# Optimization experiments

Hardware: AMD Instinct MI355X
Metric: run time of the kernel (lower is better)

Reference implementation:

```python
import jax, jax.numpy as jnp
import numpy as np

B, SL = 16, 512
S = SL - 1            # context length after shift (length=1)
E = 256               # embedding_size / hidden_size
NH = 4                # num_heads
K = 4                 # conv1d_kernel_size
I = 2 * E             # mLSTM inner dim (_inner_embedding_dim = 2*E)
DHM = I // NH         # mLSTM head dim
DHS = E // NH         # sLSTM head dim
NB, BS = I // 4, 4    # qkv_proj_blocksize=4 block-diagonal projections
F = 384               # gated FFN up dim = round_up(1.3*256, 64)
NUM_SKILLS, NUM_Q = 500, 10000
EPS = 1e-5


def _ln(x, w):
    mu = x.mean(-1, keepdims=True)
    var = x.var(-1, keepdims=True)
    return (x - mu) / jnp.sqrt(var + EPS) * w


def _causal_dwconv(x, w, b):
    # x: (B,S,C), depthwise causal conv with kernel (C,K)
    xt = jnp.transpose(x, (0, 2, 1))
    y = jax.lax.conv_general_dilated(
        xt, w[:, None, :], (1,), [(K - 1, 0)],
        dimension_numbers=('NCH', 'OIH', 'NCH'),
        feature_group_count=x.shape[-1])
    return jnp.transpose(y, (0, 2, 1)) + b


def _headwise(x, w):
    # block-diagonal linear: w (NB, BS, BS)
    xb = x.reshape(x.shape[0], x.shape[1], NB, BS)
    return jnp.einsum('bsnd,nod->bsno', xb, w).reshape(x.shape)


def _forward(questions, responses, skills,
             q_embed, qa_embed, q_embed_diff, qa_embed_diff, difficult_param,
             ln0_w, m_up_w, m_up_b, m_conv_w, m_conv_b, m_q_w, m_k_w, m_v_w,
             m_ig_w, m_ig_b, m_fg_w, m_fg_b, m_outnorm_w, m_skip, m_down_w, m_down_b,
             ln1_w, s_conv_w, s_conv_b, s_gate_w, s_rec_w, s_bias, s_gn_w,
             ln2_w, ffn_up_w, ffn_up_b, ffn_down_w, ffn_down_b,
             postnorm_w, out_w1, out_b1, out_w2, out_b2, out_w3, out_b3):
    pid = questions[:, :-1]
    q_data = skills[:, :-1]
    q_shft = skills[:, 1:]
    target = (responses * (responses > -1).astype(responses.dtype))[:, :-1]

    q_e = q_embed[q_data]                              # (B,S,E)
    qa_e = qa_embed[target] + q_e
    pid_e = difficult_param[pid]                       # (B,S,1)
    q_e = q_e + pid_e * q_embed_diff[q_data]
    qa_e = qa_e + pid_e * qa_embed_diff[target]

    # ---- xLSTM stack: block 0 = mLSTM block, block 1 = sLSTM block + gated FFN ----
    x = qa_e  # dropout is identity in eval

    # mLSTM block: x = x + mlstm_layer(LN(x))
    h = _ln(x, ln0_w)
    up = h @ m_up_w.T + m_up_b                         # (B,S,2I)
    x_m, z = jnp.split(up, 2, axis=-1)
    xc = jax.nn.silu(_causal_dwconv(x_m, m_conv_w, m_conv_b))
    q = _headwise(xc, m_q_w)
    k = _headwise(xc, m_k_w)
    v = _headwise(x_m, m_v_w)
    ifin = jnp.concatenate([q, k, v], axis=-1)         # (B,S,3I)
    ig = jnp.einsum('bsf,hf->bhs', ifin, m_ig_w) + m_ig_b[None, :, None]
    fg = jnp.einsum('bsf,hf->bhs', ifin, m_fg_w) + m_fg_b[None, :, None]
    qh = q.reshape(B, S, NH, DHM).transpose(0, 2, 1, 3)
    kh = k.reshape(B, S, NH, DHM).transpose(0, 2, 1, 3)
    vh = v.reshape(B, S, NH, DHM).transpose(0, 2, 1, 3)
    # parallel stabilized mLSTM
    logf = jax.nn.log_sigmoid(fg)                      # (B,NH,S)
    cs = jnp.concatenate([jnp.zeros((B, NH, 1), logf.dtype), jnp.cumsum(logf, -1)], -1)
    dmat = cs[:, :, 1:, None] - cs[:, :, None, 1:]     # (B,NH,S,S): sum of logf over (s,t]
    ltr = jnp.tril(jnp.ones((S, S), bool))
    logD = jnp.where(ltr, dmat, -jnp.inf) + ig[:, :, None, :]
    maxD = jnp.max(logD, -1, keepdims=True)
    D = jnp.exp(logD - maxD)
    qk = jnp.einsum('bhtd,bhsd->bhts', qh, kh) * (DHM ** -0.5)
    C = qk * D
    norm = jnp.maximum(jnp.abs(C.sum(-1, keepdims=True)), jnp.exp(-maxD))
    hh = jnp.einsum('bhts,bhsd->bhtd', C / (norm + 1e-6), vh)
    # multi-head layernorm (per head over DHM), weight on flattened dim
    hn = (hh - hh.mean(-1, keepdims=True)) / jnp.sqrt(hh.var(-1, keepdims=True) + EPS)
    hflat = hn.transpose(0, 2, 1, 3).reshape(B, S, I) * m_outnorm_w
    hout = (hflat + m_skip * xc) * jax.nn.silu(z)
    x = x + (hout @ m_down_w.T + m_down_b)

    # sLSTM block: x = x + slstm_layer(LN(x)); x = x + ffn(LN(x))
    h = _ln(x, ln1_w)
    hc = jax.nn.silu(_causal_dwconv(h, s_conv_w, s_conv_b))
    hh4 = h.reshape(B, S, NH, DHS)
    hc4 = hc.reshape(B, S, NH, DHS)
    gi = jnp.einsum('bsnd,nod->bsno', hc4, s_gate_w[0])   # i,f from conv path
    gf = jnp.einsum('bsnd,nod->bsno', hc4, s_gate_w[1])
    gz = jnp.einsum('bsnd,nod->bsno', hh4, s_gate_w[2])   # z,o from x path
    go = jnp.einsum('bsnd,nod->bsno', hh4, s_gate_w[3])
    wx = jnp.stack([gi, gf, gz, go], axis=2) + s_bias[None, None]  # (B,S,4,NH,DHS)

    def step(carry, wx_t):
        y, c, n, m = carry
        raw = wx_t + jnp.einsum('bnd,gnde->bgne', y, s_rec_w)
        iraw, fraw, zraw, oraw = raw[:, 0], raw[:, 1], raw[:, 2], raw[:, 3]
        logfplusm = m + jax.nn.log_sigmoid(fraw)
        mnew = jnp.maximum(iraw, logfplusm)
        ig_ = jnp.exp(iraw - mnew)
        fg_ = jnp.exp(logfplusm - mnew)
        cnew = fg_ * c + ig_ * jnp.tanh(zraw)
        nnew = fg_ * n + ig_
        ynew = jax.nn.sigmoid(oraw) * cnew / nnew
        return (ynew, cnew, nnew, mnew), ynew

    z0 = jnp.zeros((B, NH, DHS), x.dtype)
    _, ys = jax.lax.scan(step, (z0, z0, z0, z0), jnp.swapaxes(wx, 0, 1))
    y = jnp.swapaxes(ys, 0, 1)                           # (B,S,NH,DHS)
    yn = (y - y.mean(-1, keepdims=True)) / jnp.sqrt(y.var(-1, keepdims=True) + EPS)
    x = x + yn.reshape(B, S, E) * s_gn_w

    # gated FFN (relu)
    h = _ln(x, ln2_w)
    gate, upf = jnp.split(h @ ffn_up_w.T + ffn_up_b, 2, axis=-1)
    x = x + (jax.nn.relu(gate) * upf) @ ffn_down_w.T + ffn_down_b

    d = _ln(x, postnorm_w)                               # post_blocks_norm

    fam = jnp.where((target == 1)[..., None], d, 0.0)
    unfam = jnp.where((target == 0)[..., None], d, 0.0)
    d2 = d - pid_e
    cq = jnp.concatenate([d2, q_e, fam, unfam], axis=-1)  # (B,S,4E)
    o = jax.nn.relu(cq @ out_w1.T + out_b1)
    o = jax.nn.relu(o @ out_w2.T + out_b2)
    probs = jax.nn.sigmoid(o @ out_w3.T + out_b3)
    pred = jnp.take_along_axis(probs, q_shft[..., None], axis=-1)[..., 0]
    return pred                                          # (B,S)


def setup_inputs():
    key = jax.random.key(0)
    ks = iter(jax.random.split(key, 64))
    def rn(shape, s=0.02):
        return jax.random.normal(next(ks), shape, jnp.float32) * s
    return dict(
        questions=jax.random.randint(next(ks), (B, SL), 0, NUM_Q),
        responses=jax.random.randint(next(ks), (B, SL), 0, 2),
        skills=jax.random.randint(next(ks), (B, SL), 0, NUM_SKILLS),
        attention_mask=jnp.ones((B, SL), jnp.int32),
        q_embed=rn((NUM_SKILLS, E), 1.0),
        qa_embed=rn((2, E), 1.0),
        q_embed_diff=rn((NUM_SKILLS + 1, E), 1.0),
        qa_embed_diff=rn((2 * NUM_SKILLS + 1, E), 1.0),
        difficult_param=rn((NUM_Q + 1, 1), 0.1),
        ln0_w=jnp.ones((E,)),
        m_up_w=rn((2 * I, E)), m_up_b=jnp.zeros((2 * I,)),
        m_conv_w=rn((I, K), 0.1), m_conv_b=jnp.zeros((I,)),
        m_q_w=rn((NB, BS, BS), 0.1), m_k_w=rn((NB, BS, BS), 0.1), m_v_w=rn((NB, BS, BS), 0.1),
        m_ig_w=rn((NH, 3 * I)), m_ig_b=jnp.zeros((NH,)),
        m_fg_w=rn((NH, 3 * I)), m_fg_b=jnp.zeros((NH,)),
        m_outnorm_w=jnp.ones((I,)), m_skip=jnp.ones((I,)),
        m_down_w=rn((E, I)), m_down_b=jnp.zeros((E,)),
        ln1_w=jnp.ones((E,)),
        s_conv_w=rn((E, K), 0.1), s_conv_b=jnp.zeros((E,)),
        s_gate_w=rn((4, NH, DHS, DHS), 0.1),
        s_rec_w=rn((4, NH, DHS, DHS), 0.05),
        s_bias=jnp.zeros((4, NH, DHS)),
        s_gn_w=jnp.ones((E,)),
        ln2_w=jnp.ones((E,)),
        ffn_up_w=rn((2 * F, E)), ffn_up_b=jnp.zeros((2 * F,)),
        ffn_down_w=rn((E, F)), ffn_down_b=jnp.zeros((E,)),
        postnorm_w=jnp.ones((E,)),
        out_w1=rn((2 * E, 4 * E)), out_b1=jnp.zeros((2 * E,)),
        out_w2=rn((E, 2 * E)), out_b2=jnp.zeros((E,)),
        out_w3=rn((NUM_SKILLS, E)), out_b3=jnp.zeros((NUM_SKILLS,)),
    )


def reference(questions, responses, skills, attention_mask,
              q_embed, qa_embed, q_embed_diff, qa_embed_diff, difficult_param,
              ln0_w, m_up_w, m_up_b, m_conv_w, m_conv_b, m_q_w, m_k_w, m_v_w,
              m_ig_w, m_ig_b, m_fg_w, m_fg_b, m_outnorm_w, m_skip, m_down_w, m_down_b,
              ln1_w, s_conv_w, s_conv_b, s_gate_w, s_rec_w, s_bias, s_gn_w,
              ln2_w, ffn_up_w, ffn_up_b, ffn_down_w, ffn_down_b,
              postnorm_w, out_w1, out_b1, out_w2, out_b2, out_w3, out_b3):
    return _forward(questions, responses, skills,
                    q_embed, qa_embed, q_embed_diff, qa_embed_diff, difficult_param,
                    ln0_w, m_up_w, m_up_b, m_conv_w, m_conv_b, m_q_w, m_k_w, m_v_w,
                    m_ig_w, m_ig_b, m_fg_w, m_fg_b, m_outnorm_w, m_skip, m_down_w, m_down_b,
                    ln1_w, s_conv_w, s_conv_b, s_gate_w, s_rec_w, s_bias, s_gn_w,
                    ln2_w, ffn_up_w, ffn_up_b, ffn_down_w, ffn_down_b,
                    postnorm_w, out_w1, out_b1, out_w2, out_b2, out_w3, out_b3)
```

## Files before the change

### kernel.cpp

```cpp
#include <hip/hip_runtime.h>
#include <hip/hip_bf16.h>

#define B_    16
#define SL_   512
#define S_    511
#define E_    256
#define NH_   4
#define I_    512
#define DHM_  128
#define DHS_  64
#define F_    384
#define NP_   8192
#define NROW  (B_*S_)
#define EPS_  1e-5f

typedef __hip_bfloat16 bf16;
typedef __bf16 bf16x8v __attribute__((ext_vector_type(8)));
typedef float  f32x4v  __attribute__((ext_vector_type(4)));

__device__ __forceinline__ float rcp_(float x){ return __builtin_amdgcn_rcpf(x); }
__device__ __forceinline__ float sig_(float x){ return rcp_(1.f+__expf(-x)); }
__device__ __forceinline__ float silu_(float x){ return x*sig_(x); }
__device__ __forceinline__ float logsig_(float x){ return fminf(x,0.f) - __logf(1.f + __expf(-fabsf(x))); }
__device__ __forceinline__ float expneg_(float x){ return __expf(fminf(x,0.f)); }
__device__ __forceinline__ float expclamp_(float x){ return __expf(fminf(fmaxf(x,-80.f),80.f)); }
__device__ __forceinline__ float tanh_(float x){ return 1.f - 2.f*rcp_(__expf(2.f*x)+1.f); }

__global__ __launch_bounds__(256) void k_cvt16(const float* __restrict__ src, bf16* __restrict__ dst, int n){
  int i=blockIdx.x*256+threadIdx.x;
  if(i<n) dst[i]=__float2bfloat16(src[i]);
}
__global__ __launch_bounds__(256) void k_cvtsplit(const float* __restrict__ src,
  bf16* __restrict__ hi, bf16* __restrict__ lo, int n){
  int i=blockIdx.x*256+threadIdx.x;
  if(i<n){
    float v=src[i];
    bf16 h=__float2bfloat16(v);
    hi[i]=h;
    lo[i]=__float2bfloat16(v-__bfloat162float(h));
  }
}
__global__ __launch_bounds__(256) void k_wtrans(const float* __restrict__ src, float* __restrict__ dst){
  int i = blockIdx.x*256+threadIdx.x;
  int blk = i>>12;
  int d = (i>>6)&63;
  int e = i&63;
  dst[(size_t)(blk*64+d)*64+e] = src[(size_t)(blk*64+e)*64+d];
}

__global__ __launch_bounds__(256) void k_wfrag(const float* __restrict__ rw, bf16* __restrict__ wf){
  int i = blockIdx.x*256+threadIdx.x;
  int j  = i&7;
  int l  = (i>>3)&63;
  int kf = (i>>9)&1;
  int t  = (i>>10)&15;
  int n  = i>>14;
  int g = t>>2;
  int e = (t&3)*16 + (l&15);
  int d = (l>>4)*16 + kf*8 + j;
  wf[i] = __float2bfloat16(rw[((size_t)((g*4+n)*64 + d))*64 + e]);
}

__global__ __launch_bounds__(256) void k_embed(
  const int* __restrict__ questions, const int* __restrict__ responses, const int* __restrict__ skills,
  const float* __restrict__ q_embed, const float* __restrict__ qa_embed,
  const float* __restrict__ q_embed_diff, const float* __restrict__ qa_embed_diff,
  const float* __restrict__ difficult_param, const float* __restrict__ ln0w,
  float* __restrict__ x, float* __restrict__ qe,
  bf16* __restrict__ h_hi, bf16* __restrict__ h_lo,
  float* __restrict__ pide, int* __restrict__ tgt, int* __restrict__ qsh)
{
  __shared__ float red[256];
  int r = blockIdx.x; int e = threadIdx.x;
  float xa = 0.f;
  if (r < NROW){
    int b = r / S_, s = r % S_;
    int pid  = questions[b*SL_+s];
    int qd   = skills[b*SL_+s];
    int resp = responses[b*SL_+s];
    int t    = (resp > -1) ? resp : 0;
    float pe = difficult_param[pid];
    float q0 = q_embed[qd*E_+e];
    xa = q0 + qa_embed[t*E_+e] + pe*qa_embed_diff[t*E_+e];
    float qn = q0 + pe*q_embed_diff[qd*E_+e];
    x[(size_t)r*E_+e]=xa; qe[(size_t)r*E_+e]=qn;
    if (e==0){ pide[r]=pe; tgt[r]=t; qsh[r]=skills[b*SL_+s+1]; }
  } else {
    x[(size_t)r*E_+e]=0.f; qe[(size_t)r*E_+e]=0.f;
    if (e==0){ pide[r]=0.f; tgt[r]=-7; qsh[r]=0; }
  }
  red[e]=xa; __syncthreads();
  for(int s2=128;s2>0;s2>>=1){ if(e<s2) red[e]+=red[e+s2]; __syncthreads(); }
  float mu = red[0]*(1.f/E_); __syncthreads();
  float d = xa-mu;
  red[e]=d*d; __syncthreads();
  for(int s2=128;s2>0;s2>>=1){ if(e<s2) red[e]+=red[e+s2]; __syncthreads(); }
  float var = red[0]*(1.f/E_);
  float o = d*rsqrtf(var+EPS_)*ln0w[e];
  bf16 hv = __float2bfloat16(o);
  h_hi[(size_t)r*E_+e] = hv;
  h_lo[(size_t)r*E_+e] = __float2bfloat16(o-__bfloat162float(hv));
}

__global__ __launch_bounds__(256) void k_ln(
  const float* __restrict__ in, const float* __restrict__ w, float* __restrict__ out)
{
  __shared__ float red[256];
  int r = blockIdx.x, t = threadIdx.x;
  float v = in[(size_t)r*E_+t];
  red[t]=v; __syncthreads();
  for(int s=128;s>0;s>>=1){ if(t<s) red[t]+=red[t+s]; __syncthreads(); }
  float mu = red[0]*(1.f/E_); __syncthreads();
  float d = v-mu;
  red[t]=d*d; __syncthreads();
  for(int s=128;s>0;s>>=1){ if(t<s) red[t]+=red[t+s]; __syncthreads(); }
  float var = red[0]*(1.f/E_);
  out[(size_t)r*E_+t] = d*rsqrtf(var+EPS_)*w[t];
}

__global__ __launch_bounds__(256) void k_gemm16s(
  const bf16* __restrict__ Ah, const bf16* __restrict__ Al,
  const bf16* __restrict__ Bh, const bf16* __restrict__ Bl,
  const float* __restrict__ bias, float* __restrict__ C, int M, int K)
{
  int tid=threadIdx.x;
  int wave=tid>>6, lane=tid&63;
  int wr=wave>>1, wc=wave&1;
  int row0=blockIdx.y*64 + wr*32;
  int col0=blockIdx.x*64 + wc*32;
  int lrow = lane&15, lq = lane>>4;
  f32x4v acc[2][2] = {};
  size_t aoff = (size_t)(row0+lrow)*K + lq*8;
  size_t boff = (size_t)(col0+lrow)*K + lq*8;
  for(int k0=0;k0<K;k0+=32){
    bf16x8v ah0=*(const bf16x8v*)(Ah+aoff+k0), ah1=*(const bf16x8v*)(Ah+aoff+(size_t)16*K+k0);
    bf16x8v al0=*(const bf16x8v*)(Al+aoff+k0), al1=*(const bf16x8v*)(Al+aoff+(size_t)16*K+k0);
    bf16x8v bh0=*(const bf16x8v*)(Bh+boff+k0), bh1=*(const bf16x8v*)(Bh+boff+(size_t)16*K+k0);
    bf16x8v bl0=*(const bf16x8v*)(Bl+boff+k0), bl1=*(const bf16x8v*)(Bl+boff+(size_t)16*K+k0);
    acc[0][0]=__builtin_amdgcn_mfma_f32_16x16x32_bf16(ah0,bh0,acc[0][0],0,0,0);
    acc[0][1]=__builtin_amdgcn_mfma_f32_16x16x32_bf16(ah0,bh1,acc[0][1],0,0,0);
    acc[1][0]=__builtin_amdgcn_mfma_f32_16x16x32_bf16(ah1,bh0,acc[1][0],0,0,0);
    acc[1][1]=__builtin_amdgcn_mfma_f32_16x16x32_bf16(ah1,bh1,acc[1][1],0,0,0);
    acc[0][0]=__builtin_amdgcn_mfma_f32_16x16x32_bf16(ah0,bl0,acc[0][0],0,0,0);
    acc[0][1]=__builtin_amdgcn_mfma_f32_16x16x32_bf16(ah0,bl1,acc[0][1],0,0,0);
    acc[1][0]=__builtin_amdgcn_mfma_f32_16x16x32_bf16(ah1,bl0,acc[1][0],0,0,0);
    acc[1][1]=__builtin_amdgcn_mfma_f32_16x16x32_bf16(ah1,bl1,acc[1][1],0,0,0);
    acc[0][0]=__builtin_amdgcn_mfma_f32_16x16x32_bf16(al0,bh0,acc[0][0],0,0,0);
    acc[0][1]=__builtin_amdgcn_mfma_f32_16x16x32_bf16(al0,bh1,acc[0][1],0,0,0);
    acc[1][0]=__builtin_amdgcn_mfma_f32_16x16x32_bf16(al1,bh0,acc[1][0],0,0,0);
    acc[1][1]=__builtin_amdgcn_mfma_f32_16x16x32_bf16(al1,bh1,acc[1][1],0,0,0);
  }
  #pragma unroll
  for(int mi=0;mi<2;mi++){
    #pragma unroll
    for(int ni=0;ni<2;ni++){
      #pragma unroll
      for(int r=0;r<4;r++){
        int row=row0+mi*16+lq*4+r;
        int col=col0+ni*16+lrow;
        C[(size_t)row*M+col]=acc[mi][ni][r] + bias[col];
      }
    }
  }
}

__global__ __launch_bounds__(256) void k_gemm16(
  const bf16* __restrict__ A, const bf16* __restrict__ Bw,
  const float* __restrict__ bias, const float* __restrict__ resid,
  float* __restrict__ C, bf16* __restrict__ C16,
  int M, int K, int relu)
{
  int tid=threadIdx.x;
  int wave=tid>>6, lane=tid&63;
  int wr=wave>>1, wc=wave&1;
  int row0=blockIdx.y*64 + wr*32;
  int col0=blockIdx.x*64 + wc*32;
  int lrow = lane&15, lq = lane>>4;
  f32x4v acc[2][2] = {};
  const bf16* Abase = A  + (size_t)(row0+lrow)*K + lq*8;
  const bf16* Bbase = Bw + (size_t)(col0+lrow)*K + lq*8;
  for(int k0=0;k0<K;k0+=32){
    bf16x8v a0 = *(const bf16x8v*)(Abase + k0);
    bf16x8v a1 = *(const bf16x8v*)(Abase + (size_t)16*K + k0);
    bf16x8v b0 = *(const bf16x8v*)(Bbase + k0);
    bf16x8v b1 = *(const bf16x8v*)(Bbase + (size_t)16*K + k0);
    acc[0][0]=__builtin_amdgcn_mfma_f32_16x16x32_bf16(a0,b0,acc[0][0],0,0,0);
    acc[0][1]=__builtin_amdgcn_mfma_f32_16x16x32_bf16(a0,b1,acc[0][1],0,0,0);
    acc[1][0]=__builtin_amdgcn_mfma_f32_16x16x32_bf16(a1,b0,acc[1][0],0,0,0);
    acc[1][1]=__builtin_amdgcn_mfma_f32_16x16x32_bf16(a1,b1,acc[1][1],0,0,0);
  }
  #pragma unroll
  for(int mi=0;mi<2;mi++){
    #pragma unroll
    for(int ni=0;ni<2;ni++){
      #pragma unroll
      for(int r=0;r<4;r++){
        int row=row0+mi*16+lq*4+r;
        int col=col0+ni*16+lrow;
        float v=acc[mi][ni][r] + (bias? bias[col]:0.f);
        if(relu) v=fmaxf(v,0.f);
        if(resid) v += resid[(size_t)row*M+col];
        if(C)   C[(size_t)row*M+col]=v;
        if(C16) C16[(size_t)row*M+col]=__float2bfloat16(v);
      }
    }
  }
}

__global__ __launch_bounds__(256) void k_conv_silu(
  const float* __restrict__ in, int ild, const float* __restrict__ w, const float* __restrict__ bws,
  float* __restrict__ out, int old_, int C)
{
  int i = blockIdx.x*256 + threadIdx.x;
  int r = i / C, c = i % C;
  if (r >= NP_) return;
  float acc = 0.f;
  if (r < NROW) {
    int b=r/S_, s=r%S_;
    acc = bws[c];
    #pragma unroll
    for(int j=0;j<4;j++){
      int ss=s-3+j;
      if(ss>=0) acc += w[c*4+j] * in[(size_t)(b*S_+ss)*ild + c];
    }
    acc = silu_(acc);
  }
  out[(size_t)r*old_ + c] = acc;
}

__global__ __launch_bounds__(256) void k_headwise(
  const float* __restrict__ xc, const float* __restrict__ xm, int xmld,
  const float* __restrict__ wq, const float* __restrict__ wk, const float* __restrict__ wv,
  float* __restrict__ q, float* __restrict__ k, float* __restrict__ v)
{
  int i=blockIdx.x*256+threadIdx.x;
  int r=i/I_, c=i%I_;
  if(r>=NP_) return;
  size_t oi=(size_t)r*I_+c;
  if(r>=NROW){ q[oi]=0.f; k[oi]=0.f; v[oi]=0.f; return; }
  int n=c>>2, o=c&3;
  const float* xcr = xc + (size_t)r*I_ + n*4;
  const float* xmr = xm + (size_t)r*xmld + n*4;
  float aq=0.f, ak=0.f, av=0.f;
  #pragma unroll
  for(int d=0;d<4;d++){
    float xcv=xcr[d], xmv=xmr[d];
    aq += xcv*wq[(n*4+o)*4+d];
    ak += xcv*wk[(n*4+o)*4+d];
    av += xmv*wv[(n*4+o)*4+d];
  }
  q[oi]=aq; k[oi]=ak; v[oi]=av;
}

__global__ __launch_bounds__(256) void k_igfg(
  const float* __restrict__ q, const float* __restrict__ k, const float* __restrict__ v,
  const float* __restrict__ wig, const float* __restrict__ big,
  const float* __restrict__ wfg, const float* __restrict__ bfg,
  float* __restrict__ igb, float* __restrict__ fgb)
{
  int r=blockIdx.x;
  int wid=threadIdx.x>>6, lane=threadIdx.x&63;
  int b=r/S_, s=r%S_;
  for(int c=wid; c<8; c+=4){
    int h=c>>1; int isfg=c&1;
    const float* w = isfg? wfg : wig;
    float acc=0.f;
    for(int f=lane; f<1536; f+=64){
      float val = (f<512)? q[(size_t)r*512+f]
                : (f<1024)? k[(size_t)r*512+f-512]
                : v[(size_t)r*512+f-1024];
      acc += val*w[h*1536+f];
    }
    for(int m=32;m;m>>=1) acc+=__shfl_xor(acc,m,64);
    if(lane==0){
      if(isfg) fgb[(b*4+h)*512+s]=acc+bfg[h];
      else     igb[(b*4+h)*512+s]=acc+big[h];
    }
  }
}

__global__ __launch_bounds__(256) void k_decay(
  const float* __restrict__ igb, const float* __restrict__ fgb,
  float* __restrict__ cs1, float* __restrict__ g, float* __restrict__ M)
{
  int bh = blockIdx.x; int tid = threadIdx.x;
  __shared__ float buf[512];
  __shared__ float buf2[512];
  for (int s=tid; s<512; s+=256)
    buf[s] = (s<S_) ? logsig_(fgb[bh*512+s]) : 0.f;
  __syncthreads();
  for (int off=1; off<512; off<<=1){
    int s0=tid, s1=tid+256;
    float v0 = buf[s0] + ((s0>=off)? buf[s0-off] : 0.f);
    float v1 = buf[s1] + ((s1>=off)? buf[s1-off] : 0.f);
    __syncthreads();
    buf[s0]=v0; buf[s1]=v1;
    __syncthreads();
  }
  for (int s=tid; s<512; s+=256){
    float c = buf[s];
    if (s<S_){
      cs1[bh*512+s]=c;
      float gv = igb[bh*512+s]-c;
      g[bh*512+s]=gv;
      buf2[s]=gv;
    } else buf2[s] = -3.4e38f;
  }
  __syncthreads();
  for (int off=1; off<512; off<<=1){
    int s0=tid, s1=tid+256;
    float v0 = fmaxf(buf2[s0], (s0>=off)? buf2[s0-off] : -3.4e38f);
    float v1 = fmaxf(buf2[s1], (s1>=off)? buf2[s1-off] : -3.4e38f);
    __syncthreads();
    buf2[s0]=v0; buf2[s1]=v1;
    __syncthreads();
  }
  for (int s=tid; s<S_; s+=256) M[bh*512+s] = buf2[s];
}

#define TQ 32
#define TS 32
__global__ __launch_bounds__(256) void k_attn(
  const float* __restrict__ q, const float* __restrict__ k, const float* __restrict__ v,
  const float* __restrict__ cs1, const float* __restrict__ g, const float* __restrict__ M,
  const float* __restrict__ onw, float* __restrict__ hflat)
{
  __shared__ __align__(16) float qs[TQ][132];
  __shared__ __align__(16) float ks[TS][132];
  __shared__ __align__(16) float vs[TS][128];
  __shared__ float Sw[TQ][33];
  __shared__ float MtS[TQ], cssS[TQ], lsumS[TQ], gsS[TS];
  int tq = blockIdx.x, bh = blockIdx.y;
  int b = bh>>2, h = bh&3;
  int tid = threadIdx.x;
  int i = tid>>4, j = tid&15;
  int t0 = tq*TQ;
  {
    int row = tid>>3, c4 = (tid&7)*4;
    const float4* src = (const float4*)(q + (size_t)(b*S_ + t0 + row)*512 + h*128);
    float4* dst = (float4*)&qs[row][0];
    #pragma unroll
    for(int c=0;c<4;c++) dst[c4+c] = src[c4+c];
  }
  if (tid < TQ){
    int t = t0 + tid; int tc = (t<S_)? t : (S_-1);
    MtS[tid]  = M[bh*512 + tc];
    cssS[tid] = cs1[bh*512 + tc];
    lsumS[tid]= 0.f;
  }
  float o[2][8] = {};
  int t1 = min(t0+TQ, S_);
  int nst = (t1 + TS - 1)/TS;
  const float sc = 0.08838834764831843f;
  for (int st=0; st<nst; ++st){
    int s0 = st*TS;
    __syncthreads();
    {
      int row = tid>>3, c4 = (tid&7)*4;
      const float4* srck = (const float4*)(k + (size_t)(b*S_ + s0 + row)*512 + h*128);
      const float4* srcv = (const float4*)(v + (size_t)(b*S_ + s0 + row)*512 + h*128);
      float4* dk = (float4*)&ks[row][0];
      float4* dv = (float4*)&vs[row][0];
      #pragma unroll
      for(int c=0;c<4;c++){ dk[c4+c]=srck[c4+c]; dv[c4+c]=srcv[c4+c]; }
      if (tid < TS) gsS[tid] = g[bh*512 + s0 + tid];
    }
    __syncthreads();
    float a00=0,a01=0,a10=0,a11=0;
    {
      const float4* q0 = (const float4*)&qs[i*2][0];
      const float4* q1 = (const float4*)&qs[i*2+1][0];
      const float4* k0 = (const float4*)&ks[j][0];
      const float4* k1 = (const float4*)&ks[j+16][0];
      #pragma unroll
      for(int d4=0; d4<32; ++d4){
        float4 qa=q0[d4], qb=q1[d4], ka=k0[d4], kb=k1[d4];
        a00 += qa.x*ka.x+qa.y*ka.y+qa.z*ka.z+qa.w*ka.w;
        a01 += qa.x*kb.x+qa.y*kb.y+qa.z*kb.z+qa.w*kb.w;
        a10 += qb.x*ka.x+qb.y*ka.y+qb.z*ka.z+qb.w*ka.w;
        a11 += qb.x*kb.x+qb.y*kb.y+qb.z*kb.z+qb.w*kb.w;
      }
    }
    int tA = t0 + i*2, tB = tA+1;
    int sA = s0 + j,   sB = sA + 16;
    float gA = gsS[j], gB = gsS[j+16];
    float mA = MtS[i*2], mB = MtS[i*2+1];
    float w00 = (sA<=tA)? a00*sc*expneg_(gA-mA) : 0.f;
    float w01 = (sB<=tA)? a01*sc*expneg_(gB-mA) : 0.f;
    float w10 = (sA<=tB)? a10*sc*expneg_(gA-mB) : 0.f;
    float w11 = (sB<=tB)? a11*sc*expneg_(gB-mB) : 0.f;
    float r0 = w00+w01, r1 = w10+w11;
    #pragma unroll
    for(int msk=1; msk<16; msk<<=1){ r0 += __shfl_xor(r0,msk,16); r1 += __shfl_xor(r1,msk,16); }
    if (j==0){ lsumS[i*2] += r0; lsumS[i*2+1] += r1; }
    Sw[i*2][j]     = w00; Sw[i*2][j+16]   = w01;
    Sw[i*2+1][j]   = w10; Sw[i*2+1][j+16] = w11;
    __syncthreads();
    #pragma unroll 8
    for(int s=0;s<TS;s++){
      float w0 = Sw[i*2][s], w1 = Sw[i*2+1][s];
      float4 v0 = *(const float4*)&vs[s][j*4];
      float4 v1 = *(const float4*)&vs[s][64+j*4];
      o[0][0]+=w0*v0.x; o[0][1]+=w0*v0.y; o[0][2]+=w0*v0.z; o[0][3]+=w0*v0.w;
      o[0][4]+=w0*v1.x; o[0][5]+=w0*v1.y; o[0][6]+=w0*v1.z; o[0][7]+=w0*v1.w;
      o[1][0]+=w1*v0.x; o[1][1]+=w1*v0.y; o[1][2]+=w1*v0.z; o[1][3]+=w1*v0.w;
      o[1][4]+=w1*v1.x; o[1][5]+=w1*v1.y; o[1][6]+=w1*v1.z; o[1][7]+=w1*v1.w;
    }
  }
  __syncthreads();
  #pragma unroll
  for(int r=0;r<2;r++){
    int tl = i*2+r;
    int t = t0 + tl;
    float maxD = cssS[tl] + MtS[tl];
    float norm = fmaxf(fabsf(lsumS[tl]), expclamp_(-maxD));
    float scale = rcp_(norm+1e-6f);
    float sum=0.f;
    #pragma unroll
    for(int d=0;d<8;d++){ o[r][d]*=scale; sum+=o[r][d]; }
    #pragma unroll
    for(int msk=1; msk<16; msk<<=1) sum += __shfl_xor(sum,msk,16);
    float mu = sum*(1.f/128.f);
    float var=0.f;
    #pragma unroll
    for(int d=0;d<8;d++){ float dd=o[r][d]-mu; var+=dd*dd; }
    #pragma unroll
    for(int msk=1; msk<16; msk<<=1) var += __shfl_xor(var,msk,16);
    float rs = rsqrtf(var*(1.f/128.f)+EPS_);
    if (t < S_){
      float* dst = hflat + (size_t)(b*S_+t)*1024 + h*128;
      #pragma unroll
      for(int c=0;c<4;c++) dst[j*4+c]    = (o[r][c]  -mu)*rs*onw[h*128+j*4+c];
      #pragma unroll
      for(int c=0;c<4;c++) dst[64+j*4+c] = (o[r][4+c]-mu)*rs*onw[h*128+64+j*4+c];
    }
  }
}

__global__ __launch_bounds__(256) void k_hout(
  const float* __restrict__ A, const float* __restrict__ xc, const float* __restrict__ skip,
  bf16* __restrict__ out16)
{
  int i=blockIdx.x*256+threadIdx.x;
  int r=i/512, c=i%512;
  float hf=A[(size_t)r*1024+c];
  float z =A[(size_t)r*1024+512+c];
  out16[(size_t)r*512+c] = __float2bfloat16((hf + skip[c]*xc[(size_t)r*512+c]) * silu_(z));
}

#define WXR 64
__global__ __launch_bounds__(256,2) void k_wx(
  const float* __restrict__ h, const float* __restrict__ hc,
  const float* __restrict__ gwT, const float* __restrict__ gb,
  float* __restrict__ wx)
{
  int rt = blockIdx.x, g = blockIdx.y;
  int tid = threadIdx.x;
  int n = tid>>6, e = tid&63;
  const float* src = (g<2)? hc : h;
  __shared__ __align__(16) float hs[WXR][260];
  float W[64];
  #pragma unroll
  for(int d=0;d<64;d++) W[d] = gwT[(size_t)(((g*4+n)*64+d))*64 + e];
  float bias = gb[(g*4+n)*64+e];
  int row0 = rt*WXR;
  for(int idx=tid; idx<WXR*64; idx+=256){
    int rr = idx>>6, cc4 = (idx&63)*4;
    *(float4*)&hs[rr][cc4] = *(const float4*)(src + (size_t)(row0+rr)*256 + cc4);
  }
  __syncthreads();
  #pragma unroll 4
  for(int rr=0; rr<WXR; ++rr){
    int r = row0+rr;
    if (r>=NROW) break;
    const float* hrow = &hs[rr][n*64];
    float a0=0,a1=0,a2=0,a3=0;
    #pragma unroll
    for(int d=0;d<64;d+=4){
      float4 hv = *(const float4*)&hrow[d];
      a0+=hv.x*W[d]; a1+=hv.y*W[d+1]; a2+=hv.z*W[d+2]; a3+=hv.w*W[d+3];
    }
    int b=r/S_, s=r%S_;
    wx[(((size_t)(b*4+n)*512 + s)*256) + e*4 + g] = bias + ((a0+a1)+(a2+a3));
  }
}

__global__ __launch_bounds__(256,1) void k_scan(
  const float* __restrict__ wx, const bf16* __restrict__ wf, float* __restrict__ y_out)
{
  int bn = blockIdx.x; int b = bn>>2, n = bn&3;
  int tid = threadIdx.x;
  int w = tid>>6;
  int l = tid&63;
  int q = l>>4;
  int el = l&15;
  int e  = w*16 + el;

  __shared__ __align__(16) unsigned short ybuf[2][64];

  if (tid < 128) ((unsigned short*)ybuf)[tid] = 0;
  __syncthreads();

  bf16x8v Wf2[4][2];
  #pragma unroll
  for(int g=0; g<4; ++g){
    #pragma unroll
    for(int kf=0; kf<2; ++kf){
      Wf2[g][kf] = *(const bf16x8v*)(wf + ((size_t)((n*16 + (4*g+w))*2 + kf)*64 + l)*8);
    }
  }

  const float* wxBase = wx + ((size_t)bn*512)*256 + e*4;
  float* yst = y_out + (size_t)(b*S_)*256 + n*64 + e;

  float4 p0,p1,p2,p3;
  p0 = *(const float4*)(wxBase + (size_t)0*256);
  p1 = *(const float4*)(wxBase + (size_t)1*256);
  p2 = *(const float4*)(wxBase + (size_t)2*256);
  p3 = *(const float4*)(wxBase + (size_t)3*256);

  f32x4v z4 = {0.f,0.f,0.f,0.f};
  float c=0.f, nn=0.f, pm=1.f;

  for (int s=0; s<S_; ++s){
    int p = s&1;
    bf16x8v a0 = *(const bf16x8v*)&ybuf[p][16*q];
    bf16x8v a1 = *(const bf16x8v*)&ybuf[p][16*q+8];

    f32x4v acc0,acc1,acc2,acc3;
    acc0 = __builtin_amdgcn_mfma_f32_16x16x32_bf16(a0, Wf2[0][0], z4, 0,0,0);
    acc1 = __builtin_amdgcn_mfma_f32_16x16x32_bf16(a0, Wf2[1][0], z4, 0,0,0);
    acc2 = __builtin_amdgcn_mfma_f32_16x16x32_bf16(a0, Wf2[2][0], z4, 0,0,0);
    acc3 = __builtin_amdgcn_mfma_f32_16x16x32_bf16(a0, Wf2[3][0], z4, 0,0,0);
    acc0 = __builtin_amdgcn_mfma_f32_16x16x32_bf16(a1, Wf2[0][1], acc0, 0,0,0);
    acc1 = __builtin_amdgcn_mfma_f32_16x16x32_bf16(a1, Wf2[1][1], acc1, 0,0,0);
    acc2 = __builtin_amdgcn_mfma_f32_16x16x32_bf16(a1, Wf2[2][1], acc2, 0,0,0);
    acc3 = __builtin_amdgcn_mfma_f32_16x16x32_bf16(a1, Wf2[3][1], acc3, 0,0,0);

    float4 wg = p0; p0=p1; p1=p2; p2=p3;
    { int sp = s+4; if (sp>510) sp=510;
      p3 = *(const float4*)(wxBase + (size_t)sp*256); }

    float iraw=acc0[0]+wg.x, fraw=acc1[0]+wg.y, zraw=acc2[0]+wg.z, oraw=acc3[0]+wg.w;

    float pe  = __expf(fminf(iraw, 80.f));
    float ef  = __expf(-fraw);
    float e2z = __expf(2.f*zraw);
    float eo  = __expf(-oraw);
    float sf  = rcp_(1.f+ef);
    float ps  = pm*sf;
    float pn  = fmaxf(fmaxf(pe, ps), 1e-30f);
    float rpn = rcp_(pn);
    float fg  = ps*rpn;
    float ig  = pe*rpn;
    float th  = 1.f - 2.f*rcp_(e2z+1.f);
    c  = fg*c + ig*th;
    nn = fmaxf(fg*nn + ig, 1e-30f);
    float y = rcp_(1.f+eo) * c * rcp_(nn);
    pm = pn;

    bf16 hb = __float2bfloat16(y);
    unsigned short hbits; __builtin_memcpy(&hbits,&hb,2);
    if (l < 16){
      ybuf[p^1][e] = hbits;
      yst[(size_t)s*256] = y;
    }
    asm volatile("s_waitcnt lgkmcnt(0)" ::: "memory");
    __builtin_amdgcn_s_barrier();
    asm volatile("" ::: "memory");
    __builtin_amdgcn_sched_barrier(0);
  }
}

__global__ __launch_bounds__(256) void k_ynadd_ln2(
  const float* __restrict__ y, const float* __restrict__ gn,
  float* __restrict__ x, const float* __restrict__ ln2w, bf16* __restrict__ h16)
{
  __shared__ float red[256];
  int r=blockIdx.x, t=threadIdx.x;
  float xv = x[(size_t)r*256+t];
  if (r < NROW){
    float v=y[(size_t)r*256+t];
    float s=v;
    for(int m=32;m;m>>=1) s+=__shfl_xor(s,m,64);
    float mu=s*(1.f/64.f);
    float d=v-mu;
    float q=d*d;
    for(int m=32;m;m>>=1) q+=__shfl_xor(q,m,64);
    float var=q*(1.f/64.f);
    xv += d*rsqrtf(var+EPS_)*gn[t];
    x[(size_t)r*256+t]=xv;
  }
  red[t]=xv; __syncthreads();
  for(int s=128;s>0;s>>=1){ if(t<s) red[t]+=red[t+s]; __syncthreads(); }
  float mu2=red[0]*(1.f/E_); __syncthreads();
  float dd=xv-mu2;
  red[t]=dd*dd; __syncthreads();
  for(int s=128;s>0;s>>=1){ if(t<s) red[t]+=red[t+s]; __syncthreads(); }
  float var2=red[0]*(1.f/E_);
  h16[(size_t)r*256+t]=__float2bfloat16(dd*rsqrtf(var2+EPS_)*ln2w[t]);
}

__global__ __launch_bounds__(256) void k_ffmul(const float* __restrict__ ffu, bf16* __restrict__ out)
{
  int i=blockIdx.x*256+threadIdx.x;
  int r=i/384, j=i%384;
  out[(size_t)r*384+j] = __float2bfloat16(fmaxf(ffu[(size_t)r*768+j],0.f)*ffu[(size_t)r*768+384+j]);
}

__global__ __launch_bounds__(256) void k_cq_ln(
  const float* __restrict__ x, const float* __restrict__ pw,
  const float* __restrict__ qe, const float* __restrict__ pide, const int* __restrict__ tgt,
  bf16* __restrict__ cq)
{
  __shared__ float red[256];
  int r=blockIdx.x, t=threadIdx.x;
  float v = x[(size_t)r*256+t];
  red[t]=v; __syncthreads();
  for(int s=128;s>0;s>>=1){ if(t<s) red[t]+=red[t+s]; __syncthreads(); }
  float mu=red[0]*(1.f/E_); __syncthreads();
  float d=v-mu;
  red[t]=d*d; __syncthreads();
  for(int s=128;s>0;s>>=1){ if(t<s) red[t]+=red[t+s]; __syncthreads(); }
  float var=red[0]*(1.f/E_);
  float dv = d*rsqrtf(var+EPS_)*pw[t];
  float pe=pide[r]; int tg=tgt[r];
  size_t base=(size_t)r*1024;
  cq[base+t]=__float2bfloat16(dv-pe);
  cq[base+256+t]=__float2bfloat16(qe[(size_t)r*256+t]);
  cq[base+512+t]=__float2bfloat16((tg==1)? dv:0.f);
  cq[base+768+t]=__float2bfloat16((tg==0)? dv:0.f);
}

__global__ __launch_bounds__(256) void k_final(
  const float* __restrict__ o2, const float* __restrict__ w3, const float* __restrict__ b3,
  const int* __restrict__ qsh, float* __restrict__ out)
{
  __shared__ float red[256];
  int r=blockIdx.x, t=threadIdx.x;
  int qi=qsh[r];
  float p=o2[(size_t)r*256+t]*w3[(size_t)qi*256+t];
  red[t]=p; __syncthreads();
  for(int s=128;s>0;s>>=1){ if(t<s) red[t]+=red[t+s]; __syncthreads(); }
  if(t==0) out[r]=sig_(red[0]+b3[qi]);
}

extern "C" void kernel_launch(void* const* d_in, const int* in_sizes, int n_in,
                              void* d_out, int out_size, void* d_ws, size_t ws_size,
                              hipStream_t stream) {
  const int* questions = (const int*)d_in[0];
  const int* responses = (const int*)d_in[1];
  const int* skills    = (const int*)d_in[2];
  const float* q_embed       = (const float*)d_in[4];
  const float* qa_embed      = (const float*)d_in[5];
  const float* q_embed_diff  = (const float*)d_in[6];
  const float* qa_embed_diff = (const float*)d_in[7];
  const float* difficult_param=(const float*)d_in[8];
  const float* ln0_w   = (const float*)d_in[9];
  const float* m_up_w  = (const float*)d_in[10];
  const float* m_up_b  = (const float*)d_in[11];
  const float* m_conv_w= (const float*)d_in[12];
  const float* m_conv_b= (const float*)d_in[13];
  const float* m_q_w   = (const float*)d_in[14];
  const float* m_k_w   = (const float*)d_in[15];
  const float* m_v_w   = (const float*)d_in[16];
  const float* m_ig_w  = (const float*)d_in[17];
  const float* m_ig_b  = (const float*)d_in[18];
  const float* m_fg_w  = (const float*)d_in[19];
  const float* m_fg_b  = (const float*)d_in[20];
  const float* m_outnorm_w=(const float*)d_in[21];
  const float* m_skip  = (const float*)d_in[22];
  const float* m_down_w= (const float*)d_in[23];
  const float* m_down_b= (const float*)d_in[24];
  const float* ln1_w   = (const float*)d_in[25];
  const float* s_conv_w= (const float*)d_in[26];
  const float* s_conv_b= (const float*)d_in[27];
  const float* s_gate_w= (const float*)d_in[28];
  const float* s_rec_w = (const float*)d_in[29];
  const float* s_bias  = (const float*)d_in[30];
  const float* s_gn_w  = (const float*)d_in[31];
  const float* ln2_w   = (const float*)d_in[32];
  const float* ffn_up_w= (const float*)d_in[33];
  const float* ffn_up_b= (const float*)d_in[34];
  const float* ffn_down_w=(const float*)d_in[35];
  const float* ffn_down_b=(const float*)d_in[36];
  const float* postnorm_w=(const float*)d_in[37];
  const float* out_w1  = (const float*)d_in[38];
  const float* out_b1  = (const float*)d_in[39];
  const float* out_w2  = (const float*)d_in[40];
  const float* out_b2  = (const float*)d_in[41];
  const float* out_w3  = (const float*)d_in[42];
  const float* out_b3  = (const float*)d_in[43];

  float* ws = (float*)d_ws;
  const size_t R = (size_t)NP_*256;
  float* x    = ws;
  float* qe   = ws + R;
  float* h    = ws + 2*R;
  float* t256 = ws + 3*R;
  float* A    = ws + 4*R;
  float* Bb   = ws + 8*R;
  float* Cb   = ws + 10*R;
  float* Db   = ws + 12*R;
  float* Eb   = ws + 14*R;
  float* pide = ws + 16*R;
  int*   tgt  = (int*)(ws + 16*R + NP_);
  int*   qsh  = (int*)(ws + 16*R + 2*NP_);
  float* igb  = ws + 16*R + 3*NP_;
  float* fgb  = igb + 64*512;
  float* cs1  = fgb + 64*512;
  float* gdec = cs1 + 64*512;
  float* Mrun = gdec + 64*512;
  bf16* wpool = (bf16*)(Mrun + 64*512);
  bf16* m_down_w16  = wpool;
  bf16* ffn_up_w16  = m_down_w16 + 256*512;
  bf16* ffn_down_w16= ffn_up_w16 + 768*256;
  bf16* out_w1_16   = ffn_down_w16 + 256*384;
  bf16* out_w2_16   = out_w1_16 + 512*1024;
  bf16* h16         = out_w2_16 + 256*512;
  bf16* m_up_whi    = h16 + (size_t)NP_*256;
  bf16* m_up_wlo    = m_up_whi + 1024*256;
  float* gwT        = (float*)(m_up_wlo + 1024*256);
  bf16* wfrag       = (bf16*)(gwT + 16*64*64);
  bf16* hout16 = (bf16*)Db;
  bf16* ffg16  = (bf16*)Db;
  bf16* cq16   = (bf16*)Eb;
  bf16* b16    = (bf16*)Cb;
  bf16* h_hi   = (bf16*)t256;
  bf16* h_lo   = h_hi + (size_t)NP_*256;

  k_cvt16<<<(256*512+255)/256,256,0,stream>>>(m_down_w,  m_down_w16,  256*512);
  k_cvt16<<<(768*256+255)/256,256,0,stream>>>(ffn_up_w,  ffn_up_w16,  768*256);
  k_cvt16<<<(256*384+255)/256,256,0,stream>>>(ffn_down_w,ffn_down_w16,256*384);
  k_cvt16<<<(512*1024+255)/256,256,0,stream>>>(out_w1,   out_w1_16,   512*1024);
  k_cvt16<<<(256*512+255)/256,256,0,stream>>>(out_w2,    out_w2_16,   256*512);
  k_cvtsplit<<<(1024*256+255)/256,256,0,stream>>>(m_up_w, m_up_whi, m_up_wlo, 1024*256);
  k_wtrans<<<(16*64*64)/256,256,0,stream>>>(s_gate_w, gwT);
  k_wfrag<<<65536/256,256,0,stream>>>(s_rec_w, wfrag);

  k_embed<<<NP_,256,0,stream>>>(questions,responses,skills,q_embed,qa_embed,
      q_embed_diff,qa_embed_diff,difficult_param, ln0_w, x,qe, h_hi,h_lo, pide,tgt,qsh);
  k_gemm16s<<<dim3(1024/64,NP_/64),256,0,stream>>>(h_hi,h_lo, m_up_whi,m_up_wlo, m_up_b, A, 1024,256);
  k_conv_silu<<<(NP_*512)/256,256,0,stream>>>(A,1024, m_conv_w,m_conv_b, Bb,512,512);
  k_headwise<<<(NP_*512)/256,256,0,stream>>>(Bb, A,1024, m_q_w,m_k_w,m_v_w, Cb,Db,Eb);
  k_igfg<<<NROW,256,0,stream>>>(Cb,Db,Eb, m_ig_w,m_ig_b,m_fg_w,m_fg_b, igb,fgb);
  k_decay<<<64,256,0,stream>>>(igb,fgb, cs1,gdec,Mrun);
  k_attn<<<dim3((S_+TQ-1)/TQ, B_*NH_),256,0,stream>>>(Cb,Db,Eb, cs1,gdec,Mrun, m_outnorm_w, A);
  k_hout<<<(NP_*512)/256,256,0,stream>>>(A, Bb, m_skip, hout16);
  k_gemm16<<<dim3(256/64,NP_/64),256,0,stream>>>(hout16, m_down_w16, m_down_b, x, x, (bf16*)nullptr, 256,512,0);
  k_ln<<<NP_,256,0,stream>>>(x, ln1_w, h);
  k_conv_silu<<<(NP_*256)/256,256,0,stream>>>(h,256, s_conv_w,s_conv_b, Bb,256,256);
  k_wx<<<dim3(128,4),256,0,stream>>>(h, Bb, gwT, s_bias, A);
  k_scan<<<64,256,0,stream>>>(A, wfrag, Cb);
  k_ynadd_ln2<<<NP_,256,0,stream>>>(Cb, s_gn_w, x, ln2_w, h16);
  k_gemm16<<<dim3(768/64,NP_/64),256,0,stream>>>(h16, ffn_up_w16, ffn_up_b, (const float*)nullptr, A, (bf16*)nullptr, 768,256,0);
  k_ffmul<<<(NP_*384)/256,256,0,stream>>>(A, ffg16);
  k_gemm16<<<dim3(256/64,NP_/64),256,0,stream>>>(ffg16, ffn_down_w16, ffn_down_b, x, x, (bf16*)nullptr, 256,384,0);
  k_cq_ln<<<NP_,256,0,stream>>>(x, postnorm_w, qe, pide, tgt, cq16);
  k_gemm16<<<dim3(512/64,NP_/64),256,0,stream>>>(cq16, out_w1_16, out_b1, (const float*)nullptr, (float*)nullptr, b16, 512,1024,1);
  k_gemm16<<<dim3(256/64,NP_/64),256,0,stream>>>(b16, out_w2_16, out_b2, (const float*)nullptr, t256, (bf16*)nullptr, 256,512,1);
  k_final<<<NROW,256,0,stream>>>(t256, out_w3, out_b3, qsh, (float*)d_out);
}
```

Before: 980.8 us.

## Rewrite mLSTM attention kernel to use split-bf16 MFMA for QK and PV

The parallel mLSTM attention kernel swaps its scalar fp32 dot products for MFMA 16x16x32 bf16 instructions. Operands are split into hi and lo bf16 parts and combined with three MFMAs to keep near-fp32 accuracy. Q and K fragments are loaded straight into registers, while V and the gated weights are staged transposed in LDS as bf16. Output normalization now uses a one-pass E[x^2]-mu^2 variance, which loses some numerical robustness, and the split conversions add ALU work.

```diff
diff --git a/kernel.cpp b/kernel.cpp
--- a/kernel.cpp
+++ b/kernel.cpp
@@ -15,6 +15,7 @@
 #define EPS_  1e-5f
 
 typedef __hip_bfloat16 bf16;
+typedef unsigned short u16;
 typedef __bf16 bf16x8v __attribute__((ext_vector_type(8)));
 typedef float  f32x4v  __attribute__((ext_vector_type(4)));
 
@@ -25,6 +26,22 @@
 __device__ __forceinline__ float expneg_(float x){ return __expf(fminf(x,0.f)); }
 __device__ __forceinline__ float expclamp_(float x){ return __expf(fminf(fmaxf(x,-80.f),80.f)); }
 __device__ __forceinline__ float tanh_(float x){ return 1.f - 2.f*rcp_(__expf(2.f*x)+1.f); }
+
+__device__ __forceinline__ void cvt_split8(const float* __restrict__ p, bf16x8v& hv, bf16x8v& lv){
+  float4 u = *(const float4*)p;
+  float4 w = *(const float4*)(p+4);
+  float x[8] = {u.x,u.y,u.z,u.w,w.x,w.y,w.z,w.w};
+  union { bf16x8v v; u16 s[8]; } H, L;
+  #pragma unroll
+  for(int j=0;j<8;j++){
+    bf16 hh = __float2bfloat16(x[j]);
+    float hf = __bfloat162float(hh);
+    bf16 ll = __float2bfloat16(x[j]-hf);
+    __builtin_memcpy(&H.s[j],&hh,2);
+    __builtin_memcpy(&L.s[j],&ll,2);
+  }
+  hv=H.v; lv=L.v;
+}
 
 __global__ __launch_bounds__(256) void k_cvt16(const float* __restrict__ src, bf16* __restrict__ dst, int n){
   int i=blockIdx.x*256+threadIdx.x;
@@ -325,114 +342,182 @@
   const float* __restrict__ cs1, const float* __restrict__ g, const float* __restrict__ M,
   const float* __restrict__ onw, float* __restrict__ hflat)
 {
-  __shared__ __align__(16) float qs[TQ][132];
-  __shared__ __align__(16) float ks[TS][132];
-  __shared__ __align__(16) float vs[TS][128];
-  __shared__ float Sw[TQ][33];
-  __shared__ float MtS[TQ], cssS[TQ], lsumS[TQ], gsS[TS];
+  __shared__ __align__(16) u16 vThi[128][40];
+  __shared__ __align__(16) u16 vTlo[128][40];
+  __shared__ __align__(16) u16 phi[32][40];
+  __shared__ __align__(16) u16 plo[32][40];
+  __shared__ float MtS[32], cssS[32], normS[32], muS[32], rsS[32];
+  __shared__ float lsumW[2][32], sumA[2][32], sumB[2][32];
+
   int tq = blockIdx.x, bh = blockIdx.y;
   int b = bh>>2, h = bh&3;
   int tid = threadIdx.x;
-  int i = tid>>4, j = tid&15;
+  int wv = tid>>6;
+  int tw = wv&1, sw = wv>>1;
+  int l = tid&63;
+  int lr = l&15, lg = l>>4;
   int t0 = tq*TQ;
-  {
-    int row = tid>>3, c4 = (tid&7)*4;
-    const float4* src = (const float4*)(q + (size_t)(b*S_ + t0 + row)*512 + h*128);
-    float4* dst = (float4*)&qs[row][0];
-    #pragma unroll
-    for(int c=0;c<4;c++) dst[c4+c] = src[c4+c];
-  }
-  if (tid < TQ){
+  const float sc = 0.08838834764831843f;
+
+  if (tid < 32){
     int t = t0 + tid; int tc = (t<S_)? t : (S_-1);
     MtS[tid]  = M[bh*512 + tc];
     cssS[tid] = cs1[bh*512 + tc];
-    lsumS[tid]= 0.f;
-  }
-  float o[2][8] = {};
+  }
+
+  bf16x8v qh[4], ql[4];
+  {
+    const float* qrow = q + ((size_t)(b*S_ + t0 + tw*16 + lr))*512 + h*128 + lg*8;
+    #pragma unroll
+    for(int k0=0;k0<4;k0++) cvt_split8(qrow + (size_t)k0*32, qh[k0], ql[k0]);
+  }
+
+  f32x4v accpv[4] = {};
+  float lsum[4] = {0.f,0.f,0.f,0.f};
+
   int t1 = min(t0+TQ, S_);
-  int nst = (t1 + TS - 1)/TS;
-  const float sc = 0.08838834764831843f;
-  for (int st=0; st<nst; ++st){
-    int s0 = st*TS;
+  int sp = tid>>4, dl = tid&15;
+
+  __syncthreads();
+
+  for (int s0=0; s0<t1; s0+=TS){
+    bf16x8v kh[4], kl2[4];
+    {
+      const float* krow = k + ((size_t)(b*S_ + s0 + sw*16 + lr))*512 + h*128 + lg*8;
+      #pragma unroll
+      for(int k0=0;k0<4;k0++) cvt_split8(krow + (size_t)k0*32, kh[k0], kl2[k0]);
+    }
+    float va[8], vb[8];
+    {
+      const float* vap = v + ((size_t)(b*S_ + s0 + 2*sp))*512 + h*128 + dl;
+      const float* vbp = vap + 512;
+      #pragma unroll
+      for(int j=0;j<8;j++){ va[j]=vap[16*j]; vb[j]=vbp[16*j]; }
+    }
+    float g_s = g[bh*512 + s0 + sw*16 + lr];
+
+    f32x4v cqk = {0.f,0.f,0.f,0.f};
+    #pragma unroll
+    for(int k0=0;k0<4;k0++){
+      cqk = __builtin_amdgcn_mfma_f32_16x16x32_bf16(qh[k0], kh[k0],  cqk, 0,0,0);
+      cqk = __builtin_amdgcn_mfma_f32_16x16x32_bf16(qh[k0], kl2[k0], cqk, 0,0,0);
+      cqk = __builtin_amdgcn_mfma_f32_16x16x32_bf16(ql[k0], kh[k0],  cqk, 0,0,0);
+    }
+
+    int s_g = s0 + sw*16 + lr;
+    u16 pw_h[4], pw_l[4];
+    #pragma unroll
+    for(int r=0;r<4;r++){
+      int tl = tw*16 + lg*4 + r;
+      int t_row = t0 + tl;
+      float wvv = ((s_g <= t_row) && (t_row < S_)) ? cqk[r]*sc*expneg_(g_s - MtS[tl]) : 0.f;
+      lsum[r] += wvv;
+      bf16 hh = __float2bfloat16(wvv);
+      float hf = __bfloat162float(hh);
+      bf16 ll = __float2bfloat16(wvv - hf);
+      __builtin_memcpy(&pw_h[r], &hh, 2);
+      __builtin_memcpy(&pw_l[r], &ll, 2);
+    }
+
     __syncthreads();
+
+    #pragma unroll
+    for(int r=0;r<4;r++){
+      int tl = tw*16 + lg*4 + r;
+      phi[tl][sw*16 + lr] = pw_h[r];
+      plo[tl][sw*16 + lr] = pw_l[r];
+    }
     {
-      int row = tid>>3, c4 = (tid&7)*4;
-      const float4* srck = (const float4*)(k + (size_t)(b*S_ + s0 + row)*512 + h*128);
-      const float4* srcv = (const float4*)(v + (size_t)(b*S_ + s0 + row)*512 + h*128);
-      float4* dk = (float4*)&ks[row][0];
-      float4* dv = (float4*)&vs[row][0];
+      unsigned* vh32 = (unsigned*)&vThi[0][0];
+      unsigned* vl32 = (unsigned*)&vTlo[0][0];
       #pragma unroll
-      for(int c=0;c<4;c++){ dk[c4+c]=srck[c4+c]; dv[c4+c]=srcv[c4+c]; }
-      if (tid < TS) gsS[tid] = g[bh*512 + s0 + tid];
-    }
+      for(int j=0;j<8;j++){
+        int d = dl + 16*j;
+        bf16 ha=__float2bfloat16(va[j]);
+        bf16 hb=__float2bfloat16(vb[j]);
+        float haf=__bfloat162float(ha), hbf=__bfloat162float(hb);
+        bf16 la=__float2bfloat16(va[j]-haf);
+        bf16 lb=__float2bfloat16(vb[j]-hbf);
+        u16 hau,hbu,lau,lbu;
+        __builtin_memcpy(&hau,&ha,2); __builtin_memcpy(&hbu,&hb,2);
+        __builtin_memcpy(&lau,&la,2); __builtin_memcpy(&lbu,&lb,2);
+        vh32[d*20 + sp] = (unsigned)hau | ((unsigned)hbu<<16);
+        vl32[d*20 + sp] = (unsigned)lau | ((unsigned)lbu<<16);
+      }
+    }
+
     __syncthreads();
-    float a00=0,a01=0,a10=0,a11=0;
-    {
-      const float4* q0 = (const float4*)&qs[i*2][0];
-      const float4* q1 = (const float4*)&qs[i*2+1][0];
-      const float4* k0 = (const float4*)&ks[j][0];
-      const float4* k1 = (const float4*)&ks[j+16][0];
-      #pragma unroll
-      for(int d4=0; d4<32; ++d4){
-        float4 qa=q0[d4], qb=q1[d4], ka=k0[d4], kb=k1[d4];
-        a00 += qa.x*ka.x+qa.y*ka.y+qa.z*ka.z+qa.w*ka.w;
-        a01 += qa.x*kb.x+qa.y*kb.y+qa.z*kb.z+qa.w*kb.w;
-        a10 += qb.x*ka.x+qb.y*ka.y+qb.z*ka.z+qb.w*ka.w;
-        a11 += qb.x*kb.x+qb.y*kb.y+qb.z*kb.z+qb.w*kb.w;
-      }
-    }
-    int tA = t0 + i*2, tB = tA+1;
-    int sA = s0 + j,   sB = sA + 16;
-    float gA = gsS[j], gB = gsS[j+16];
-    float mA = MtS[i*2], mB = MtS[i*2+1];
-    float w00 = (sA<=tA)? a00*sc*expneg_(gA-mA) : 0.f;
-    float w01 = (sB<=tA)? a01*sc*expneg_(gB-mA) : 0.f;
-    float w10 = (sA<=tB)? a10*sc*expneg_(gA-mB) : 0.f;
-    float w11 = (sB<=tB)? a11*sc*expneg_(gB-mB) : 0.f;
-    float r0 = w00+w01, r1 = w10+w11;
-    #pragma unroll
-    for(int msk=1; msk<16; msk<<=1){ r0 += __shfl_xor(r0,msk,16); r1 += __shfl_xor(r1,msk,16); }
-    if (j==0){ lsumS[i*2] += r0; lsumS[i*2+1] += r1; }
-    Sw[i*2][j]     = w00; Sw[i*2][j+16]   = w01;
-    Sw[i*2+1][j]   = w10; Sw[i*2+1][j+16] = w11;
-    __syncthreads();
-    #pragma unroll 8
-    for(int s=0;s<TS;s++){
-      float w0 = Sw[i*2][s], w1 = Sw[i*2+1][s];
-      float4 v0 = *(const float4*)&vs[s][j*4];
-      float4 v1 = *(const float4*)&vs[s][64+j*4];
-      o[0][0]+=w0*v0.x; o[0][1]+=w0*v0.y; o[0][2]+=w0*v0.z; o[0][3]+=w0*v0.w;
-      o[0][4]+=w0*v1.x; o[0][5]+=w0*v1.y; o[0][6]+=w0*v1.z; o[0][7]+=w0*v1.w;
-      o[1][0]+=w1*v0.x; o[1][1]+=w1*v0.y; o[1][2]+=w1*v0.z; o[1][3]+=w1*v0.w;
-      o[1][4]+=w1*v1.x; o[1][5]+=w1*v1.y; o[1][6]+=w1*v1.z; o[1][7]+=w1*v1.w;
-    }
+
+    bf16x8v pah = *(const bf16x8v*)((const void*)(&phi[tw*16 + lr][0] + lg*8));
+    bf16x8v pal = *(const bf16x8v*)((const void*)(&plo[tw*16 + lr][0] + lg*8));
+    #pragma unroll
+    for(int fd=0; fd<4; fd++){
+      bf16x8v vbh = *(const bf16x8v*)((const void*)(&vThi[sw*64 + fd*16 + lr][0] + lg*8));
+      bf16x8v vbl = *(const bf16x8v*)((const void*)(&vTlo[sw*64 + fd*16 + lr][0] + lg*8));
+      accpv[fd] = __builtin_amdgcn_mfma_f32_16x16x32_bf16(pah, vbh, accpv[fd], 0,0,0);
+      accpv[fd] = __builtin_amdgcn_mfma_f32_16x16x32_bf16(pah, vbl, accpv[fd], 0,0,0);
+      accpv[fd] = __builtin_amdgcn_mfma_f32_16x16x32_bf16(pal, vbh, accpv[fd], 0,0,0);
+    }
+  }
+
+  #pragma unroll
+  for(int r=0;r<4;r++){
+    #pragma unroll
+    for(int m=1;m<16;m<<=1) lsum[r] += __shfl_xor(lsum[r], m, 16);
+  }
+  if (lr==0){
+    #pragma unroll
+    for(int r=0;r<4;r++) lsumW[sw][tw*16 + lg*4 + r] = lsum[r];
   }
   __syncthreads();
-  #pragma unroll
-  for(int r=0;r<2;r++){
-    int tl = i*2+r;
-    int t = t0 + tl;
-    float maxD = cssS[tl] + MtS[tl];
-    float norm = fmaxf(fabsf(lsumS[tl]), expclamp_(-maxD));
-    float scale = rcp_(norm+1e-6f);
-    float sum=0.f;
-    #pragma unroll
-    for(int d=0;d<8;d++){ o[r][d]*=scale; sum+=o[r][d]; }
-    #pragma unroll
-    for(int msk=1; msk<16; msk<<=1) sum += __shfl_xor(sum,msk,16);
-    float mu = sum*(1.f/128.f);
-    float var=0.f;
-    #pragma unroll
-    for(int d=0;d<8;d++){ float dd=o[r][d]-mu; var+=dd*dd; }
-    #pragma unroll
-    for(int msk=1; msk<16; msk<<=1) var += __shfl_xor(var,msk,16);
-    float rs = rsqrtf(var*(1.f/128.f)+EPS_);
-    if (t < S_){
-      float* dst = hflat + (size_t)(b*S_+t)*1024 + h*128;
-      #pragma unroll
-      for(int c=0;c<4;c++) dst[j*4+c]    = (o[r][c]  -mu)*rs*onw[h*128+j*4+c];
-      #pragma unroll
-      for(int c=0;c<4;c++) dst[64+j*4+c] = (o[r][4+c]-mu)*rs*onw[h*128+64+j*4+c];
+  if (tid < 32){
+    float ls = lsumW[0][tid] + lsumW[1][tid];
+    float maxD = cssS[tid] + MtS[tid];
+    float nrm = fmaxf(fabsf(ls), expclamp_(-maxD));
+    normS[tid] = rcp_(nrm + 1e-6f);
+  }
+  __syncthreads();
+
+  float o_[4][4];
+  float srow[4]={0.f,0.f,0.f,0.f}, sq[4]={0.f,0.f,0.f,0.f};
+  #pragma unroll
+  for(int r=0;r<4;r++){
+    float scl = normS[tw*16 + lg*4 + r];
+    #pragma unroll
+    for(int fd=0;fd<4;fd++){
+      float o = accpv[fd][r]*scl;
+      o_[fd][r] = o;
+      srow[r] += o; sq[r] += o*o;
+    }
+  }
+  #pragma unroll
+  for(int r=0;r<4;r++){
+    #pragma unroll
+    for(int m=1;m<16;m<<=1){ srow[r]+=__shfl_xor(srow[r],m,16); sq[r]+=__shfl_xor(sq[r],m,16); }
+  }
+  if (lr==0){
+    #pragma unroll
+    for(int r=0;r<4;r++){ sumA[sw][tw*16+lg*4+r]=srow[r]; sumB[sw][tw*16+lg*4+r]=sq[r]; }
+  }
+  __syncthreads();
+  if (tid < 32){
+    float mu = (sumA[0][tid]+sumA[1][tid])*(1.f/128.f);
+    float ex2= (sumB[0][tid]+sumB[1][tid])*(1.f/128.f);
+    muS[tid]=mu;
+    rsS[tid]=rsqrtf(fmaxf(ex2 - mu*mu, 0.f)+EPS_);
+  }
+  __syncthreads();
+
+  #pragma unroll
+  for(int fd=0; fd<4; fd++){
+    int d = sw*64 + fd*16 + lr;
+    float ow = onw[h*128 + d];
+    #pragma unroll
+    for(int r=0;r<4;r++){
+      int tl = tw*16 + lg*4 + r;
+      int t = t0 + tl;
+      if (t < S_)
+        hflat[((size_t)(b*S_+t))*1024 + h*128 + d] = (o_[fd][r]-muS[tl])*rsS[tl]*ow;
     }
   }
 }
```

Measured after the change: 879.2 us. 10.4% less time.
